# Kernel tuning notes

Hardware: AMD Instinct MI355X
Metric: run time of the kernel (lower is better)

Reference implementation:

```python
import jax, jax.numpy as jnp
import numpy as np

B = 2048        # graphs per batch
NC = 81         # cells per sudoku
IN_C, HID = 10, 128
N_ACT, N_NUM, N_TECH = 4, 9, 10


def _sudoku_edges():
    idx = np.arange(NC).reshape(9, 9)
    adj = np.zeros((NC, NC), dtype=bool)
    for i in range(9):
        for j in range(9):
            n = idx[i, j]
            adj[n, idx[i, :]] = True
            adj[n, idx[:, j]] = True
            bi, bj = 3 * (i // 3), 3 * (j // 3)
            adj[n, idx[bi:bi + 3, bj:bj + 3].reshape(-1)] = True
            adj[n, n] = False
    src, dst = np.nonzero(adj)  # 1620 directed edges
    return np.stack([src, dst]).astype(np.int32)


def setup_inputs() -> dict:
    key = jax.random.key(0)
    ks = jax.random.split(key, 12)
    N = B * NC
    base = _sudoku_edges()                          # [2, 1620]
    offs = (np.arange(B, dtype=np.int32) * NC)      # [B]
    ei = (base[:, None, :] + offs[None, :, None]).reshape(2, -1)  # [2, B*1620]
    batch = np.repeat(np.arange(B, dtype=np.int32), NC)           # [N]

    def lin(k, fan_in, fan_out):
        s = 1.0 / np.sqrt(fan_in)
        return jax.random.uniform(k, (fan_in, fan_out), jnp.float32, -s, s)

    return {
        "x": jax.random.normal(ks[0], (N, IN_C), jnp.float32),
        "edge_index": jnp.asarray(ei),
        "batch": jnp.asarray(batch),
        "W1": lin(ks[1], IN_C, HID), "b1": jnp.zeros((HID,), jnp.float32),
        "W2": lin(ks[2], HID, HID),  "b2": jnp.zeros((HID,), jnp.float32),
        "Wa": lin(ks[3], HID, N_ACT),  "ba": jnp.zeros((N_ACT,), jnp.float32),
        "Wc": lin(ks[4], HID, NC),     "bc": jnp.zeros((NC,), jnp.float32),
        "Wn": lin(ks[5], HID, N_NUM),  "bn": jnp.zeros((N_NUM,), jnp.float32),
        "Wt": lin(ks[6], HID, N_TECH), "bt": jnp.zeros((N_TECH,), jnp.float32),
    }


def _gcn_conv(x, edge_index, W, b):
    n = x.shape[0]
    loop = jnp.arange(n, dtype=edge_index.dtype)
    src = jnp.concatenate([edge_index[0], loop])
    dst = jnp.concatenate([edge_index[1], loop])
    deg = jax.ops.segment_sum(jnp.ones_like(dst, jnp.float32), dst, num_segments=n)
    dinv = jax.lax.rsqrt(deg)            # deg >= 1 due to self-loops
    norm = dinv[src] * dinv[dst]         # [E+N]
    h = x @ W                            # [N, out]
    msg = h[src] * norm[:, None]         # gather + scale
    return jax.ops.segment_sum(msg, dst, num_segments=n) + b


def reference(x, edge_index, batch, W1, b1, W2, b2, Wa, ba, Wc, bc, Wn, bn, Wt, bt):
    h = jax.nn.relu(_gcn_conv(x, edge_index, W1, b1))
    h = jax.nn.relu(_gcn_conv(h, edge_index, W2, b2))
    # global mean pool over graphs
    sums = jax.ops.segment_sum(h, batch, num_segments=B)
    cnts = jax.ops.segment_sum(jnp.ones((h.shape[0],), h.dtype), batch, num_segments=B)
    pooled = sums / jnp.maximum(cnts, 1.0)[:, None]   # [B, HID]
    return (pooled @ Wa + ba, pooled @ Wc + bc, pooled @ Wn + bn, pooled @ Wt + bt)
```

## Files before the change

### kernel.cpp

```cpp
#include <hip/hip_runtime.h>
#include <hip/hip_bf16.h>

typedef __attribute__((ext_vector_type(8))) short bf16x8;
typedef __attribute__((ext_vector_type(4))) float f32x4;

__device__ __forceinline__ unsigned short f2b(float f) {
    __hip_bfloat16 h = __float2bfloat16(f);
    return __builtin_bit_cast(unsigned short, h);
}
__device__ __forceinline__ float b2f(unsigned short u) {
    unsigned v = ((unsigned)u) << 16;
    return __builtin_bit_cast(float, v);
}
__device__ __forceinline__ float ldf(const void* p, int idx, bool f32) {
    return f32 ? ((const float*)p)[idx] : b2f(((const unsigned short*)p)[idx]);
}
__device__ __forceinline__ unsigned short ldb(const void* p, int idx, bool f32) {
    return f32 ? f2b(((const float*)p)[idx]) : ((const unsigned short*)p)[idx];
}

#define WS_FLAG   0
#define WS_B1F    16
#define WS_B2F    528
#define WS_BHF    1040
#define WS_W1R    1536
#define WS_W2R    9728
#define WS_SR     42496
#define WS_WH     60928

__global__ void k_detect(const unsigned short* __restrict__ x, int* __restrict__ flag) {
    int lane = threadIdx.x;
    int wild = 0;
#pragma unroll
    for (int i = 0; i < 4; ++i) {
        unsigned e = (x[lane * 4 + i] >> 7) & 0xFF;
        if (e != 0 && (e < 0x68 || e > 0x90)) ++wild;
    }
#pragma unroll
    for (int off = 32; off; off >>= 1) wild += __shfl_down(wild, off);
    if (lane == 0) *flag = (wild > 32) ? 1 : 0;
}

__global__ void k_repack(const void* __restrict__ W1, const void* __restrict__ b1,
                         const void* __restrict__ W2, const void* __restrict__ b2,
                         const void* __restrict__ Wa, const void* __restrict__ ba,
                         const void* __restrict__ Wc, const void* __restrict__ bc,
                         const void* __restrict__ Wn, const void* __restrict__ bn,
                         const void* __restrict__ Wt, const void* __restrict__ bt,
                         char* __restrict__ ws) {
    const bool f32 = (*(const int*)(ws + WS_FLAG)) != 0;
    int idx = blockIdx.x * blockDim.x + threadIdx.x;
    if (idx < 4096) {
        int f = idx >> 5, k = idx & 31;
        unsigned short v = (k < 10) ? ldb(W1, k * 128 + f, f32) : (unsigned short)0;
        ((unsigned short*)(ws + WS_W1R))[idx] = v;
        return;
    }
    idx -= 4096;
    if (idx < 16384) {
        int f = idx >> 7, k = idx & 127;
        ((unsigned short*)(ws + WS_W2R))[idx] = ldb(W2, k * 128 + f, f32);
        return;
    }
    idx -= 16384;
    if (idx < 9216) {
        int fi = idx >> 9, rem = idx & 511;
        int lane = rem >> 3, j = rem & 7;
        int mi = fi / 3, kc = fi - mi * 3;
        int node = mi * 16 + (lane & 15);
        int cell = kc * 32 + ((lane >> 4) << 3) + j;
        bool adj = false;
        if (node < 81 && cell < 81) {
            int ni = node / 9, nj = node % 9;
            int ci = cell / 9, cj = cell % 9;
            adj = (ni == ci) || (nj == cj) ||
                  ((ni / 3 == ci / 3) && (nj / 3 == cj / 3));
        }
        ((unsigned short*)(ws + WS_SR))[idx] = adj ? (unsigned short)0x3F80 : (unsigned short)0;
        return;
    }
    idx -= 9216;
    if (idx < 13312) {
        int o = idx >> 7, f = idx & 127;
        const void* W; int oo, dim;
        if (o < 4)       { W = Wa; oo = o;      dim = 4;  }
        else if (o < 85) { W = Wc; oo = o - 4;  dim = 81; }
        else if (o < 94) { W = Wn; oo = o - 85; dim = 9;  }
        else             { W = Wt; oo = o - 94; dim = 10; }
        ((float*)(ws + WS_WH))[idx] = ldf(W, f * dim + oo, f32);
        return;
    }
    idx -= 13312;
    if (idx < 360) {
        float v;
        if (idx < 128)      v = ldf(b1, idx, f32);
        else if (idx < 256) v = ldf(b2, idx - 128, f32);
        else {
            int o = idx - 256;
            if (o < 4)       v = ldf(ba, o, f32);
            else if (o < 85) v = ldf(bc, o - 4, f32);
            else if (o < 94) v = ldf(bn, o - 85, f32);
            else             v = ldf(bt, o - 94, f32);
        }
        if (idx < 128)      ((float*)(ws + WS_B1F))[idx] = v;
        else if (idx < 256) ((float*)(ws + WS_B2F))[idx - 128] = v;
        else                ((float*)(ws + WS_BHF))[idx - 256] = v;
    }
}

#define SAT_STRIDE 104
#define SH_STRIDE  136

__global__ __launch_bounds__(256, 2) void sudoku_gnn(
    const void* __restrict__ x, const char* __restrict__ ws,
    void* __restrict__ out, int nB)
{
    __shared__ __attribute__((aligned(16))) unsigned short sAT[128 * SAT_STRIDE];
    __shared__ __attribute__((aligned(16))) unsigned short sH [96  * SH_STRIDE ];
    __shared__ __attribute__((aligned(16))) unsigned int   xs[816];
    __shared__ float sPoolPart[256];
    __shared__ float sPool[128];

    const bool f32 = (*(const int*)(ws + WS_FLAG)) != 0;
    const unsigned short* w1r = (const unsigned short*)(ws + WS_W1R);
    const unsigned short* w2r = (const unsigned short*)(ws + WS_W2R);
    const unsigned short* sr  = (const unsigned short*)(ws + WS_SR);
    const float* b1f = (const float*)(ws + WS_B1F);
    const float* b2f = (const float*)(ws + WS_B2F);
    const float* bhf = (const float*)(ws + WS_BHF);
    const float* whf = (const float*)(ws + WS_WH);

    const int tid  = threadIdx.x;
    const int wave = tid >> 6;
    const int lane = tid & 63;
    const int ln15 = lane & 15;
    const int q    = lane >> 4;
    const int k0   = q * 8;
    const int mtb  = (wave & 1) * 3;
    const int fb   = (wave >> 1) * 64;
    const int g    = blockIdx.x;

    {
        const int words = f32 ? 810 : 405;
        const unsigned int* src = (const unsigned int*)x + (size_t)g * words;
        for (int i = tid; i < words; i += 256) xs[i] = src[i];
    }

    bf16x8 sfr[3][3];
#pragma unroll
    for (int kc = 0; kc < 3; ++kc)
#pragma unroll
        for (int mt = 0; mt < 3; ++mt) {
            int mi = mtb + mt;
            sfr[kc][mt] = *(const bf16x8*)&sr[((mi * 3 + kc) * 64 + lane) * 8];
        }
    bf16x8 w1f[4];
#pragma unroll
    for (int nt = 0; nt < 4; ++nt) {
        int f = fb + nt * 16 + ln15;
        w1f[nt] = *(const bf16x8*)&w1r[f * 32 + k0];
    }

    for (int idx = tid; idx < 15 * SH_STRIDE; idx += 256) sH[81 * SH_STRIDE + idx] = 0;
    __syncthreads();

    bf16x8 xf[3];
#pragma unroll
    for (int mt = 0; mt < 3; ++mt) {
        int node = (mtb + mt) * 16 + ln15;
        bf16x8 v = {0, 0, 0, 0, 0, 0, 0, 0};
        if (node < 81) {
            if (q == 0) {
#pragma unroll
                for (int jj = 0; jj < 8; ++jj)
                    v[jj] = (short)(f32 ? f2b(((const float*)xs)[node * 10 + jj])
                                        : ((const unsigned short*)xs)[node * 10 + jj]);
            } else if (q == 1) {
#pragma unroll
                for (int jj = 0; jj < 2; ++jj)
                    v[jj] = (short)(f32 ? f2b(((const float*)xs)[node * 10 + 8 + jj])
                                        : ((const unsigned short*)xs)[node * 10 + 8 + jj]);
            }
        }
        xf[mt] = v;
    }

    const f32x4 z4 = {0.f, 0.f, 0.f, 0.f};
    f32x4 acc[3][4];

#pragma unroll
    for (int mt = 0; mt < 3; ++mt)
#pragma unroll
        for (int nt = 0; nt < 4; ++nt)
            acc[mt][nt] = __builtin_amdgcn_mfma_f32_16x16x32_bf16(xf[mt], w1f[nt], z4, 0, 0, 0);
#pragma unroll
    for (int mt = 0; mt < 3; ++mt)
#pragma unroll
        for (int nt = 0; nt < 4; ++nt) {
            int f = fb + nt * 16 + ln15;
            int nodeb = (mtb + mt) * 16 + q * 4;
            unsigned lo = (unsigned)f2b(acc[mt][nt][0]) | ((unsigned)f2b(acc[mt][nt][1]) << 16);
            unsigned hi = (unsigned)f2b(acc[mt][nt][2]) | ((unsigned)f2b(acc[mt][nt][3]) << 16);
            *(uint2*)&sAT[f * SAT_STRIDE + nodeb] = make_uint2(lo, hi);
        }
    __syncthreads();

#pragma unroll
    for (int mt = 0; mt < 3; ++mt)
#pragma unroll
        for (int nt = 0; nt < 4; ++nt) acc[mt][nt] = z4;
#pragma unroll
    for (int kc = 0; kc < 3; ++kc) {
        bf16x8 bt4[4];
#pragma unroll
        for (int nt = 0; nt < 4; ++nt)
            bt4[nt] = *(const bf16x8*)&sAT[(fb + nt * 16 + ln15) * SAT_STRIDE + kc * 32 + k0];
#pragma unroll
        for (int mt = 0; mt < 3; ++mt)
#pragma unroll
            for (int nt = 0; nt < 4; ++nt)
                acc[mt][nt] = __builtin_amdgcn_mfma_f32_16x16x32_bf16(sfr[kc][mt], bt4[nt], acc[mt][nt], 0, 0, 0);
    }
#pragma unroll
    for (int nt = 0; nt < 4; ++nt) {
        int f = fb + nt * 16 + ln15;
        float bv = b1f[f];
#pragma unroll
        for (int mt = 0; mt < 3; ++mt) {
            int nodeb = (mtb + mt) * 16 + q * 4;
#pragma unroll
            for (int r = 0; r < 4; ++r) {
                int node = nodeb + r;
                if (node < 81) {
                    float h = fmaxf(acc[mt][nt][r] * (1.0f / 21.0f) + bv, 0.0f);
                    sH[node * SH_STRIDE + f] = f2b(h);
                }
            }
        }
    }
    __syncthreads();

#pragma unroll
    for (int mt = 0; mt < 3; ++mt)
#pragma unroll
        for (int nt = 0; nt < 4; ++nt) acc[mt][nt] = z4;
#pragma unroll
    for (int kc = 0; kc < 4; ++kc) {
        bf16x8 w2f[4];
#pragma unroll
        for (int nt = 0; nt < 4; ++nt)
            w2f[nt] = *(const bf16x8*)&w2r[(fb + nt * 16 + ln15) * 128 + kc * 32 + k0];
        bf16x8 at3[3];
#pragma unroll
        for (int mt = 0; mt < 3; ++mt)
            at3[mt] = *(const bf16x8*)&sH[((mtb + mt) * 16 + ln15) * SH_STRIDE + kc * 32 + k0];
#pragma unroll
        for (int mt = 0; mt < 3; ++mt)
#pragma unroll
            for (int nt = 0; nt < 4; ++nt)
                acc[mt][nt] = __builtin_amdgcn_mfma_f32_16x16x32_bf16(at3[mt], w2f[nt], acc[mt][nt], 0, 0, 0);
    }
#pragma unroll
    for (int mt = 0; mt < 3; ++mt)
#pragma unroll
        for (int nt = 0; nt < 4; ++nt) {
            int f = fb + nt * 16 + ln15;
            int nodeb = (mtb + mt) * 16 + q * 4;
            unsigned lo = (unsigned)f2b(acc[mt][nt][0]) | ((unsigned)f2b(acc[mt][nt][1]) << 16);
            unsigned hi = (unsigned)f2b(acc[mt][nt][2]) | ((unsigned)f2b(acc[mt][nt][3]) << 16);
            *(uint2*)&sAT[f * SAT_STRIDE + nodeb] = make_uint2(lo, hi);
        }
    __syncthreads();

#pragma unroll
    for (int mt = 0; mt < 3; ++mt)
#pragma unroll
        for (int nt = 0; nt < 4; ++nt) acc[mt][nt] = z4;
#pragma unroll
    for (int kc = 0; kc < 3; ++kc) {
        bf16x8 bt4[4];
#pragma unroll
        for (int nt = 0; nt < 4; ++nt)
            bt4[nt] = *(const bf16x8*)&sAT[(fb + nt * 16 + ln15) * SAT_STRIDE + kc * 32 + k0];
#pragma unroll
        for (int mt = 0; mt < 3; ++mt)
#pragma unroll
            for (int nt = 0; nt < 4; ++nt)
                acc[mt][nt] = __builtin_amdgcn_mfma_f32_16x16x32_bf16(sfr[kc][mt], bt4[nt], acc[mt][nt], 0, 0, 0);
    }
#pragma unroll
    for (int nt = 0; nt < 4; ++nt) {
        int f = fb + nt * 16 + ln15;
        float bv = b2f[f];
        float p = 0.f;
#pragma unroll
        for (int mt = 0; mt < 3; ++mt) {
            int nodeb = (mtb + mt) * 16 + q * 4;
#pragma unroll
            for (int r = 0; r < 4; ++r) {
                int node = nodeb + r;
                if (node < 81)
                    p += fmaxf(acc[mt][nt][r] * (1.0f / 21.0f) + bv, 0.0f);
            }
        }
        p += __shfl_down(p, 32);
        p += __shfl_down(p, 16);
        if (lane < 16) sPoolPart[(wave & 1) * 128 + f] = p;
    }
    __syncthreads();
    if (tid < 128) sPool[tid] = (sPoolPart[tid] + sPoolPart[128 + tid]) / 81.0f;
    __syncthreads();

    if (tid < 104) {
        float a = bhf[tid];
        const float4* wrow = (const float4*)(whf + tid * 128);
#pragma unroll 8
        for (int i = 0; i < 32; ++i) {
            float4 wv = wrow[i];
            a += sPool[i * 4 + 0] * wv.x + sPool[i * 4 + 1] * wv.y +
                 sPool[i * 4 + 2] * wv.z + sPool[i * 4 + 3] * wv.w;
        }
        int o = tid, oo; size_t off;
        if (o < 4)       { oo = o;      off = (size_t)g * 4 + oo; }
        else if (o < 85) { oo = o - 4;  off = (size_t)nB * 4  + (size_t)g * 81 + oo; }
        else if (o < 94) { oo = o - 85; off = (size_t)nB * 85 + (size_t)g * 9  + oo; }
        else             { oo = o - 94; off = (size_t)nB * 94 + (size_t)g * 10 + oo; }
        if (f32) ((float*)out)[off] = a;
        else     ((unsigned short*)out)[off] = f2b(a);
    }
}

extern "C" void kernel_launch(void* const* d_in, const int* in_sizes, int n_in,
                              void* d_out, int out_size, void* d_ws, size_t ws_size,
                              hipStream_t stream) {
    const void* x  = d_in[0];
    int nB = in_sizes[2] / 81;
    if (nB <= 0) return;

    char* ws = (char*)d_ws;
    hipLaunchKernelGGL(k_detect, dim3(1), dim3(64), 0, stream,
                       (const unsigned short*)x, (int*)(ws + WS_FLAG));
    hipLaunchKernelGGL(k_repack, dim3(170), dim3(256), 0, stream,
                       d_in[3], d_in[4], d_in[5], d_in[6],
                       d_in[7], d_in[8], d_in[9], d_in[10],
                       d_in[11], d_in[12], d_in[13], d_in[14], ws);
    hipLaunchKernelGGL(sudoku_gnn, dim3(nB), dim3(256), 0, stream,
                       x, (const char*)ws, d_out, nB);
}
```

Before: 156.8 us.

## Merge LDS buffers, transpose aggregation MFMA, inline dtype sniff, raise occupancy

Merges the two shared-memory tiles into one reused buffer, cutting LDS per block so that four blocks per CU can be resident (launch bounds raised to 4). The neighbor-aggregation MFMAs are transposed so each lane holds four consecutive features, which allows vectorized bias loads, packed uint2 stores of H, and xor-shuffle pooling with float4 stores. The separate dtype-detect kernel is removed and each kernel sniffs the input itself, saving one launch. Extra barriers are added to protect the shared buffer, and the higher occupancy target may force register spills.

```diff
diff --git a/kernel.cpp b/kernel.cpp
--- a/kernel.cpp
+++ b/kernel.cpp
@@ -19,7 +19,17 @@
     return f32 ? f2b(((const float*)p)[idx]) : ((const unsigned short*)p)[idx];
 }
 
-#define WS_FLAG   0
+__device__ __forceinline__ bool sniff_f32(const void* x) {
+    const unsigned* p = (const unsigned*)x;
+    int wild = 0;
+#pragma unroll
+    for (int i = 0; i < 16; ++i) {
+        unsigned e = (p[i] >> 7) & 0xFF;
+        wild += (e != 0 && (e < 0x68 || e > 0x90)) ? 1 : 0;
+    }
+    return wild > 8;
+}
+
 #define WS_B1F    16
 #define WS_B2F    528
 #define WS_BHF    1040
@@ -28,27 +38,15 @@
 #define WS_SR     42496
 #define WS_WH     60928
 
-__global__ void k_detect(const unsigned short* __restrict__ x, int* __restrict__ flag) {
-    int lane = threadIdx.x;
-    int wild = 0;
-#pragma unroll
-    for (int i = 0; i < 4; ++i) {
-        unsigned e = (x[lane * 4 + i] >> 7) & 0xFF;
-        if (e != 0 && (e < 0x68 || e > 0x90)) ++wild;
-    }
-#pragma unroll
-    for (int off = 32; off; off >>= 1) wild += __shfl_down(wild, off);
-    if (lane == 0) *flag = (wild > 32) ? 1 : 0;
-}
-
-__global__ void k_repack(const void* __restrict__ W1, const void* __restrict__ b1,
+__global__ void k_repack(const void* __restrict__ x,
+                         const void* __restrict__ W1, const void* __restrict__ b1,
                          const void* __restrict__ W2, const void* __restrict__ b2,
                          const void* __restrict__ Wa, const void* __restrict__ ba,
                          const void* __restrict__ Wc, const void* __restrict__ bc,
                          const void* __restrict__ Wn, const void* __restrict__ bn,
                          const void* __restrict__ Wt, const void* __restrict__ bt,
                          char* __restrict__ ws) {
-    const bool f32 = (*(const int*)(ws + WS_FLAG)) != 0;
+    const bool f32 = sniff_f32(x);
     int idx = blockIdx.x * blockDim.x + threadIdx.x;
     if (idx < 4096) {
         int f = idx >> 5, k = idx & 31;
@@ -108,20 +106,19 @@
     }
 }
 
-#define SAT_STRIDE 104
-#define SH_STRIDE  136
-
-__global__ __launch_bounds__(256, 2) void sudoku_gnn(
+#define T_STRIDE 104
+#define H_STRIDE 136
+
+__global__ __launch_bounds__(256, 4) void sudoku_gnn(
     const void* __restrict__ x, const char* __restrict__ ws,
     void* __restrict__ out, int nB)
 {
-    __shared__ __attribute__((aligned(16))) unsigned short sAT[128 * SAT_STRIDE];
-    __shared__ __attribute__((aligned(16))) unsigned short sH [96  * SH_STRIDE ];
+    __shared__ __attribute__((aligned(16))) unsigned short sBuf[13312];
     __shared__ __attribute__((aligned(16))) unsigned int   xs[816];
     __shared__ float sPoolPart[256];
     __shared__ float sPool[128];
 
-    const bool f32 = (*(const int*)(ws + WS_FLAG)) != 0;
+    const bool f32 = sniff_f32(x);
     const unsigned short* w1r = (const unsigned short*)(ws + WS_W1R);
     const unsigned short* w2r = (const unsigned short*)(ws + WS_W2R);
     const unsigned short* sr  = (const unsigned short*)(ws + WS_SR);
@@ -137,8 +134,10 @@
     const int q    = lane >> 4;
     const int k0   = q * 8;
     const int mtb  = (wave & 1) * 3;
+    const int nb   = (wave & 1) * 48;
     const int fb   = (wave >> 1) * 64;
     const int g    = blockIdx.x;
+    const float inv21 = 1.0f / 21.0f;
 
     {
         const int words = f32 ? 810 : 405;
@@ -150,18 +149,13 @@
 #pragma unroll
     for (int kc = 0; kc < 3; ++kc)
 #pragma unroll
-        for (int mt = 0; mt < 3; ++mt) {
-            int mi = mtb + mt;
-            sfr[kc][mt] = *(const bf16x8*)&sr[((mi * 3 + kc) * 64 + lane) * 8];
-        }
+        for (int jt = 0; jt < 3; ++jt)
+            sfr[kc][jt] = *(const bf16x8*)&sr[(((mtb + jt) * 3 + kc) * 64 + lane) * 8];
     bf16x8 w1f[4];
 #pragma unroll
-    for (int nt = 0; nt < 4; ++nt) {
-        int f = fb + nt * 16 + ln15;
-        w1f[nt] = *(const bf16x8*)&w1r[f * 32 + k0];
-    }
-
-    for (int idx = tid; idx < 15 * SH_STRIDE; idx += 256) sH[81 * SH_STRIDE + idx] = 0;
+    for (int nt = 0; nt < 4; ++nt)
+        w1f[nt] = *(const bf16x8*)&w1r[(fb + nt * 16 + ln15) * 32 + k0];
+
     __syncthreads();
 
     bf16x8 xf[3];
@@ -201,41 +195,40 @@
             int nodeb = (mtb + mt) * 16 + q * 4;
             unsigned lo = (unsigned)f2b(acc[mt][nt][0]) | ((unsigned)f2b(acc[mt][nt][1]) << 16);
             unsigned hi = (unsigned)f2b(acc[mt][nt][2]) | ((unsigned)f2b(acc[mt][nt][3]) << 16);
-            *(uint2*)&sAT[f * SAT_STRIDE + nodeb] = make_uint2(lo, hi);
-        }
-    __syncthreads();
-
-#pragma unroll
-    for (int mt = 0; mt < 3; ++mt)
-#pragma unroll
-        for (int nt = 0; nt < 4; ++nt) acc[mt][nt] = z4;
+            *(uint2*)&sBuf[f * T_STRIDE + nodeb] = make_uint2(lo, hi);
+        }
+    __syncthreads();
+
+#pragma unroll
+    for (int at = 0; at < 3; ++at)
+#pragma unroll
+        for (int jt = 0; jt < 4; ++jt) acc[at][jt] = z4;
 #pragma unroll
     for (int kc = 0; kc < 3; ++kc) {
-        bf16x8 bt4[4];
-#pragma unroll
-        for (int nt = 0; nt < 4; ++nt)
-            bt4[nt] = *(const bf16x8*)&sAT[(fb + nt * 16 + ln15) * SAT_STRIDE + kc * 32 + k0];
-#pragma unroll
-        for (int mt = 0; mt < 3; ++mt)
-#pragma unroll
-            for (int nt = 0; nt < 4; ++nt)
-                acc[mt][nt] = __builtin_amdgcn_mfma_f32_16x16x32_bf16(sfr[kc][mt], bt4[nt], acc[mt][nt], 0, 0, 0);
-    }
-#pragma unroll
-    for (int nt = 0; nt < 4; ++nt) {
-        int f = fb + nt * 16 + ln15;
-        float bv = b1f[f];
-#pragma unroll
-        for (int mt = 0; mt < 3; ++mt) {
-            int nodeb = (mtb + mt) * 16 + q * 4;
-#pragma unroll
-            for (int r = 0; r < 4; ++r) {
-                int node = nodeb + r;
-                if (node < 81) {
-                    float h = fmaxf(acc[mt][nt][r] * (1.0f / 21.0f) + bv, 0.0f);
-                    sH[node * SH_STRIDE + f] = f2b(h);
-                }
-            }
+        bf16x8 a4[4];
+#pragma unroll
+        for (int at = 0; at < 4; ++at)
+            a4[at] = *(const bf16x8*)&sBuf[(fb + at * 16 + ln15) * T_STRIDE + kc * 32 + k0];
+#pragma unroll
+        for (int at = 0; at < 4; ++at)
+#pragma unroll
+            for (int jt = 0; jt < 3; ++jt)
+                acc[jt][at] = __builtin_amdgcn_mfma_f32_16x16x32_bf16(a4[at], sfr[kc][jt], acc[jt][at], 0, 0, 0);
+    }
+    __syncthreads();
+#pragma unroll
+    for (int at = 0; at < 4; ++at) {
+        float4 bv = *(const float4*)&b1f[fb + at * 16 + q * 4];
+#pragma unroll
+        for (int jt = 0; jt < 3; ++jt) {
+            int node = nb + jt * 16 + ln15;
+            float v0 = fmaxf(acc[jt][at][0] * inv21 + bv.x, 0.0f);
+            float v1 = fmaxf(acc[jt][at][1] * inv21 + bv.y, 0.0f);
+            float v2 = fmaxf(acc[jt][at][2] * inv21 + bv.z, 0.0f);
+            float v3 = fmaxf(acc[jt][at][3] * inv21 + bv.w, 0.0f);
+            unsigned lo = (unsigned)f2b(v0) | ((unsigned)f2b(v1) << 16);
+            unsigned hi = (unsigned)f2b(v2) | ((unsigned)f2b(v3) << 16);
+            *(uint2*)&sBuf[node * H_STRIDE + fb + at * 16 + q * 4] = make_uint2(lo, hi);
         }
     }
     __syncthreads();
@@ -250,16 +243,17 @@
 #pragma unroll
         for (int nt = 0; nt < 4; ++nt)
             w2f[nt] = *(const bf16x8*)&w2r[(fb + nt * 16 + ln15) * 128 + kc * 32 + k0];
-        bf16x8 at3[3];
+        bf16x8 a3[3];
 #pragma unroll
         for (int mt = 0; mt < 3; ++mt)
-            at3[mt] = *(const bf16x8*)&sH[((mtb + mt) * 16 + ln15) * SH_STRIDE + kc * 32 + k0];
+            a3[mt] = *(const bf16x8*)&sBuf[((mtb + mt) * 16 + ln15) * H_STRIDE + kc * 32 + k0];
 #pragma unroll
         for (int mt = 0; mt < 3; ++mt)
 #pragma unroll
             for (int nt = 0; nt < 4; ++nt)
-                acc[mt][nt] = __builtin_amdgcn_mfma_f32_16x16x32_bf16(at3[mt], w2f[nt], acc[mt][nt], 0, 0, 0);
-    }
+                acc[mt][nt] = __builtin_amdgcn_mfma_f32_16x16x32_bf16(a3[mt], w2f[nt], acc[mt][nt], 0, 0, 0);
+    }
+    __syncthreads();
 #pragma unroll
     for (int mt = 0; mt < 3; ++mt)
 #pragma unroll
@@ -268,44 +262,51 @@
             int nodeb = (mtb + mt) * 16 + q * 4;
             unsigned lo = (unsigned)f2b(acc[mt][nt][0]) | ((unsigned)f2b(acc[mt][nt][1]) << 16);
             unsigned hi = (unsigned)f2b(acc[mt][nt][2]) | ((unsigned)f2b(acc[mt][nt][3]) << 16);
-            *(uint2*)&sAT[f * SAT_STRIDE + nodeb] = make_uint2(lo, hi);
-        }
-    __syncthreads();
-
-#pragma unroll
-    for (int mt = 0; mt < 3; ++mt)
-#pragma unroll
-        for (int nt = 0; nt < 4; ++nt) acc[mt][nt] = z4;
+            *(uint2*)&sBuf[f * T_STRIDE + nodeb] = make_uint2(lo, hi);
+        }
+    __syncthreads();
+
+#pragma unroll
+    for (int at = 0; at < 3; ++at)
+#pragma unroll
+        for (int jt = 0; jt < 4; ++jt) acc[at][jt] = z4;
 #pragma unroll
     for (int kc = 0; kc < 3; ++kc) {
-        bf16x8 bt4[4];
-#pragma unroll
-        for (int nt = 0; nt < 4; ++nt)
-            bt4[nt] = *(const bf16x8*)&sAT[(fb + nt * 16 + ln15) * SAT_STRIDE + kc * 32 + k0];
-#pragma unroll
-        for (int mt = 0; mt < 3; ++mt)
-#pragma unroll
-            for (int nt = 0; nt < 4; ++nt)
-                acc[mt][nt] = __builtin_amdgcn_mfma_f32_16x16x32_bf16(sfr[kc][mt], bt4[nt], acc[mt][nt], 0, 0, 0);
-    }
-#pragma unroll
-    for (int nt = 0; nt < 4; ++nt) {
-        int f = fb + nt * 16 + ln15;
-        float bv = b2f[f];
-        float p = 0.f;
-#pragma unroll
-        for (int mt = 0; mt < 3; ++mt) {
-            int nodeb = (mtb + mt) * 16 + q * 4;
-#pragma unroll
-            for (int r = 0; r < 4; ++r) {
-                int node = nodeb + r;
-                if (node < 81)
-                    p += fmaxf(acc[mt][nt][r] * (1.0f / 21.0f) + bv, 0.0f);
+        bf16x8 a4[4];
+#pragma unroll
+        for (int at = 0; at < 4; ++at)
+            a4[at] = *(const bf16x8*)&sBuf[(fb + at * 16 + ln15) * T_STRIDE + kc * 32 + k0];
+#pragma unroll
+        for (int at = 0; at < 4; ++at)
+#pragma unroll
+            for (int jt = 0; jt < 3; ++jt)
+                acc[jt][at] = __builtin_amdgcn_mfma_f32_16x16x32_bf16(a4[at], sfr[kc][jt], acc[jt][at], 0, 0, 0);
+    }
+#pragma unroll
+    for (int at = 0; at < 4; ++at) {
+        float4 bv = *(const float4*)&b2f[fb + at * 16 + q * 4];
+        float s0 = 0.f, s1 = 0.f, s2 = 0.f, s3 = 0.f;
+#pragma unroll
+        for (int jt = 0; jt < 3; ++jt) {
+            int node = nb + jt * 16 + ln15;
+            if (node < 81) {
+                s0 += fmaxf(acc[jt][at][0] * inv21 + bv.x, 0.0f);
+                s1 += fmaxf(acc[jt][at][1] * inv21 + bv.y, 0.0f);
+                s2 += fmaxf(acc[jt][at][2] * inv21 + bv.z, 0.0f);
+                s3 += fmaxf(acc[jt][at][3] * inv21 + bv.w, 0.0f);
             }
         }
-        p += __shfl_down(p, 32);
-        p += __shfl_down(p, 16);
-        if (lane < 16) sPoolPart[(wave & 1) * 128 + f] = p;
+#pragma unroll
+        for (int off = 1; off < 16; off <<= 1) {
+            s0 += __shfl_xor(s0, off);
+            s1 += __shfl_xor(s1, off);
+            s2 += __shfl_xor(s2, off);
+            s3 += __shfl_xor(s3, off);
+        }
+        if (ln15 == 0) {
+            float4 v = {s0, s1, s2, s3};
+            *(float4*)&sPoolPart[(wave & 1) * 128 + fb + at * 16 + q * 4] = v;
+        }
     }
     __syncthreads();
     if (tid < 128) sPool[tid] = (sPoolPart[tid] + sPoolPart[128 + tid]) / 81.0f;
@@ -314,11 +315,12 @@
     if (tid < 104) {
         float a = bhf[tid];
         const float4* wrow = (const float4*)(whf + tid * 128);
+        const float4* sp4  = (const float4*)sPool;
 #pragma unroll 8
         for (int i = 0; i < 32; ++i) {
             float4 wv = wrow[i];
-            a += sPool[i * 4 + 0] * wv.x + sPool[i * 4 + 1] * wv.y +
-                 sPool[i * 4 + 2] * wv.z + sPool[i * 4 + 3] * wv.w;
+            float4 pv = sp4[i];
+            a += pv.x * wv.x + pv.y * wv.y + pv.z * wv.z + pv.w * wv.w;
         }
         int o = tid, oo; size_t off;
         if (o < 4)       { oo = o;      off = (size_t)g * 4 + oo; }
@@ -338,10 +340,8 @@
     if (nB <= 0) return;
 
     char* ws = (char*)d_ws;
-    hipLaunchKernelGGL(k_detect, dim3(1), dim3(64), 0, stream,
-                       (const unsigned short*)x, (int*)(ws + WS_FLAG));
     hipLaunchKernelGGL(k_repack, dim3(170), dim3(256), 0, stream,
-                       d_in[3], d_in[4], d_in[5], d_in[6],
+                       x, d_in[3], d_in[4], d_in[5], d_in[6],
                        d_in[7], d_in[8], d_in[9], d_in[10],
                        d_in[11], d_in[12], d_in[13], d_in[14], ws);
     hipLaunchKernelGGL(sudoku_gnn, dim3(nB), dim3(256), 0, stream,
```

New measurement: 147.6 us. 5.9% less time.
